# Kernel tuning notes

Hardware: AMD Instinct MI355X
Metric: run time of the kernel (lower is better)

The kernel has to match this reference:

```python
import jax, jax.numpy as jnp
import numpy as np

D = 1024      # input_dim / embed_dim
H = 1024      # hidden_dim
H2 = H // 2
M = 15        # n_masks
NH = 4        # n_heads
B = 8192
LN_EPS = 1e-5


def setup_inputs() -> dict:
    key = jax.random.key(0)
    ks = jax.random.split(key, 16)
    s = 0.02
    return {
        "x": jax.random.normal(ks[0], (B, D), jnp.float32),
        # nn.MultiheadAttention params (torch layout: y = x @ W.T + b)
        "in_proj_w": jax.random.normal(ks[1], (3 * D, D), jnp.float32) * s,
        "in_proj_b": jax.random.normal(ks[2], (3 * D,), jnp.float32) * s,
        "out_proj_w": jax.random.normal(ks[3], (D, D), jnp.float32) * s,
        "out_proj_b": jax.random.normal(ks[4], (D,), jnp.float32) * s,
        # 15 mask MLPs stacked along leading axis (grouped GEMM form)
        "W1": jax.random.normal(ks[5], (M, D, H), jnp.float32) * s,
        "b1": jax.random.normal(ks[6], (M, H), jnp.float32) * s,
        "ln_g": jnp.ones((M, H), jnp.float32),
        "ln_b": jnp.zeros((M, H), jnp.float32),
        "W2": jax.random.normal(ks[7], (M, H, H2), jnp.float32) * s,
        "b2": jax.random.normal(ks[8], (M, H2), jnp.float32) * s,
        "W3": jax.random.normal(ks[9], (M, H2, D), jnp.float32) * s,
        "b3": jax.random.normal(ks[10], (M, D), jnp.float32) * s,
    }


def reference(x, in_proj_w, in_proj_b, out_proj_w, out_proj_b,
              W1, b1, ln_g, ln_b, W2, b2, W3, b3):
    Bn = x.shape[0]
    hd = D // NH
    # --- seq_len=1 self-attention ---
    qkv = x @ in_proj_w.T + in_proj_b                      # [B, 3D]
    q, k, v = jnp.split(qkv, 3, axis=-1)                   # each [B, D]
    qh = q.reshape(Bn, NH, hd)
    kh = k.reshape(Bn, NH, hd)
    vh = v.reshape(Bn, NH, hd)
    scores = jnp.sum(qh * kh, axis=-1) / jnp.sqrt(jnp.float32(hd))  # [B, NH]
    # softmax over kv length = 1 -> all ones (kept for faithfulness)
    w = jax.nn.softmax(scores[..., None], axis=-1)         # [B, NH, 1]
    attn = (w * vh).reshape(Bn, D)                         # [B, D]
    a = attn @ out_proj_w.T + out_proj_b                   # [B, D]
    # --- 15 mask MLPs as one grouped GEMM stack (Dropout is eval->identity) ---
    h1 = jnp.einsum('bd,mdh->mbh', a, W1) + b1[:, None, :]  # [M, B, H]
    mu = jnp.mean(h1, axis=-1, keepdims=True)
    var = jnp.mean(jnp.square(h1 - mu), axis=-1, keepdims=True)
    h1 = (h1 - mu) * jax.lax.rsqrt(var + LN_EPS) * ln_g[:, None, :] + ln_b[:, None, :]
    h1 = jax.nn.gelu(h1, approximate=False)
    h2 = jnp.einsum('mbh,mhk->mbk', h1, W2) + b2[:, None, :]  # [M, B, H2]
    h2 = jax.nn.gelu(h2, approximate=False)
    h3 = jnp.einsum('mbk,mkd->mbd', h2, W3) + b3[:, None, :]  # [M, B, D]
    return jax.nn.sigmoid(h3)                               # [M, B, D]
```

## Files before the change

### kernel.cpp

```cpp
#include <hip/hip_runtime.h>

#define D_  1024
#define H_  1024
#define H2_ 512
#define M_  15
#define B_  8192

typedef __attribute__((ext_vector_type(4))) float f32x4;
typedef __attribute__((ext_vector_type(8))) short short8;

__device__ __forceinline__ unsigned short f2bf(float f) {
  unsigned int u = __float_as_uint(f);
  u += 0x7fffu + ((u >> 16) & 1u);
  return (unsigned short)(u >> 16);
}
__device__ __forceinline__ float bf2f(unsigned int h) {
  return __uint_as_float(h << 16);
}
__device__ __forceinline__ float gelu_exact(float x) {
  return 0.5f * x * (1.0f + erff(x * 0.70710678118654752440f));
}

__global__ void cast_f32_bf16(const float* __restrict__ in, unsigned short* __restrict__ out, int n4) {
  int i = blockIdx.x * blockDim.x + threadIdx.x;
  if (i >= n4) return;
  float4 v = ((const float4*)in)[i];
  ushort4 o;
  o.x = f2bf(v.x); o.y = f2bf(v.y); o.z = f2bf(v.z); o.w = f2bf(v.w);
  ((ushort4*)out)[i] = o;
}

__global__ void transpose_cast(const float* __restrict__ in, unsigned short* __restrict__ out,
                               int K, int N) {
  __shared__ float t[32][33];
  const size_t mo = (size_t)blockIdx.z * K * N;
  in  += mo;
  out += mo;
  const int k0 = blockIdx.x * 32, n0 = blockIdx.y * 32;
  const int tx = threadIdx.x, ty = threadIdx.y;
#pragma unroll
  for (int j = 0; j < 32; j += 8)
    t[ty + j][tx] = in[(size_t)(k0 + ty + j) * N + (n0 + tx)];
  __syncthreads();
#pragma unroll
  for (int j = 0; j < 32; j += 8)
    out[(size_t)(n0 + ty + j) * K + (k0 + tx)] = f2bf(t[tx][ty + j]);
}

template <int EPI>
__launch_bounds__(256, 3)
__global__ void gemm_bt(const unsigned short* __restrict__ A, const unsigned short* __restrict__ Bt,
                        const float* __restrict__ bias, void* __restrict__ Cout,
                        int Mrows, int N, int K,
                        long sA, long sB, long sBias, long sC) {
  __shared__ __align__(16) unsigned short As[128 * 64];
  __shared__ __align__(16) unsigned short Bs[128 * 64];
  const int mz = blockIdx.z;
  A    += (size_t)mz * sA;
  Bt   += (size_t)mz * sB;
  bias += (size_t)mz * sBias;

  const int tid  = threadIdx.x;
  const int w    = tid >> 6;
  const int lane = tid & 63;
  const int row0 = blockIdx.x * 128;
  const int col0 = blockIdx.y * 128;

  f32x4 acc[4][4];
#pragma unroll
  for (int i = 0; i < 4; ++i)
#pragma unroll
    for (int j = 0; j < 4; ++j) acc[i][j] = (f32x4){0.f, 0.f, 0.f, 0.f};

  const int wm = w >> 1, wn = w & 1;
  const int mrow = lane & 15;
  const int kq   = (lane >> 4) << 3;

  for (int k0 = 0; k0 < K; k0 += 64) {
    __syncthreads();
#pragma unroll
    for (int i = 0; i < 4; ++i) {
      const int c  = i * 256 + tid;
      const int m  = c >> 3;
      const int kk = (c & 7) << 3;
      const unsigned short* gA = A  + (size_t)(row0 + m) * K + (k0 + kk);
      const unsigned short* gB = Bt + (size_t)(col0 + m) * K + (k0 + kk);
      const int ldsoff = (i * 256 + w * 64) * 8;
      __builtin_amdgcn_global_load_lds((const __attribute__((address_space(1))) void*)gA,
                                       (__attribute__((address_space(3))) void*)(As + ldsoff),
                                       16, 0, 0);
      __builtin_amdgcn_global_load_lds((const __attribute__((address_space(1))) void*)gB,
                                       (__attribute__((address_space(3))) void*)(Bs + ldsoff),
                                       16, 0, 0);
    }
    __syncthreads();
#pragma unroll
    for (int ki = 0; ki < 64; ki += 32) {
      short8 af[4], bf[4];
#pragma unroll
      for (int f = 0; f < 4; ++f) {
        af[f] = *(const short8*)(As + (wm * 64 + f * 16 + mrow) * 64 + ki + kq);
        bf[f] = *(const short8*)(Bs + (wn * 64 + f * 16 + mrow) * 64 + ki + kq);
      }
#pragma unroll
      for (int fm = 0; fm < 4; ++fm)
#pragma unroll
        for (int fn = 0; fn < 4; ++fn)
          acc[fm][fn] = __builtin_amdgcn_mfma_f32_16x16x32_bf16(af[fm], bf[fn], acc[fm][fn], 0, 0, 0);
    }
  }

  float*          Cf = (float*)Cout          + (size_t)mz * sC;
  unsigned short* Cb = (unsigned short*)Cout + (size_t)mz * sC;
  const int rq = (lane >> 4) << 2;
  const int cl = lane & 15;
#pragma unroll
  for (int fm = 0; fm < 4; ++fm) {
#pragma unroll
    for (int fn = 0; fn < 4; ++fn) {
      const int cc = col0 + wn * 64 + fn * 16 + cl;
      const float bv = bias[cc];
#pragma unroll
      for (int r = 0; r < 4; ++r) {
        const int rr = row0 + wm * 64 + fm * 16 + rq + r;
        float v = acc[fm][fn][r] + bv;
        if (EPI == 2) {
          Cf[(size_t)rr * N + cc] = 1.0f / (1.0f + __expf(-v));
        } else {
          if (EPI == 1) v = gelu_exact(v);
          Cb[(size_t)rr * N + cc] = f2bf(v);
        }
      }
    }
  }
}

#define BAR()   asm volatile("s_barrier" ::: "memory")
#define LGKM0() asm volatile("s_waitcnt lgkmcnt(0)" ::: "memory")
#define VM6()   asm volatile("s_waitcnt vmcnt(6)" ::: "memory")

#define STG_A(bufi, bA, rho0) do {                                                             \
  _Pragma("unroll")                                                                            \
  for (int j_ = 0; j_ < 2; ++j_) {                                                             \
    const int rho_ = (rho0) + j_ * 64 + (tid >> 3);                                            \
    const int gr_  = (((rho_ >> 6) & 1) << 7) | (((rho_ >> 7) & 1) << 6) | (rho_ & 63);        \
    const unsigned short* g_ = (bA) + (size_t)gr_ * K + (((tid & 7) ^ (rho_ & 7)) << 3);       \
    __builtin_amdgcn_global_load_lds((const __attribute__((address_space(1))) void*)g_,        \
        (__attribute__((address_space(3))) void*)(&As[bufi][(rho0) * 64 + (j_ * 512 + w6 * 64) * 8]), \
        16, 0, 0);                                                                             \
  }                                                                                            \
} while (0)

#define STG_B(bufi, bB, rho0) do {                                                             \
  _Pragma("unroll")                                                                            \
  for (int j_ = 0; j_ < 2; ++j_) {                                                             \
    const int rho_ = (rho0) + j_ * 64 + (tid >> 3);                                            \
    const int gc_  = (((rho_ >> 5) & 3) << 6) | (((rho_ >> 7) & 1) << 5) | (rho_ & 31);        \
    const unsigned short* g_ = (bB) + (size_t)gc_ * K + (((tid & 7) ^ (rho_ & 7)) << 3);       \
    __builtin_amdgcn_global_load_lds((const __attribute__((address_space(1))) void*)g_,        \
        (__attribute__((address_space(3))) void*)(&Bs[bufi][(rho0) * 64 + (j_ * 512 + w6 * 64) * 8]), \
        16, 0, 0);                                                                             \
  }                                                                                            \
} while (0)

#define LDA4(bufi, hi) do {                                                                    \
  _Pragma("unroll")                                                                            \
  for (int q_ = 0; q_ < 4; ++q_) {                                                             \
    const int rho_ = ((hi) ? 128 : 0) + wm * 64 + q_ * 16 + lrow;                              \
    a[q_][0] = *(const short8*)&As[bufi][rho_ * 64 + ((lk ^ (rho_ & 7)) << 3)];                \
    a[q_][1] = *(const short8*)&As[bufi][rho_ * 64 + (((4 + lk) ^ (rho_ & 7)) << 3)];          \
  }                                                                                            \
} while (0)

#define LDB2(bufi, hi) do {                                                                    \
  _Pragma("unroll")                                                                            \
  for (int q_ = 0; q_ < 2; ++q_) {                                                             \
    const int rho_ = ((hi) ? 128 : 0) + wn * 32 + q_ * 16 + lrow;                              \
    b[(hi) * 2 + q_][0] = *(const short8*)&Bs[bufi][rho_ * 64 + ((lk ^ (rho_ & 7)) << 3)];     \
    b[(hi) * 2 + q_][1] = *(const short8*)&Bs[bufi][rho_ * 64 + (((4 + lk) ^ (rho_ & 7)) << 3)]; \
  }                                                                                            \
} while (0)

#define MMQ(mh, nh) do {                                                                       \
  __builtin_amdgcn_s_setprio(1);                                                               \
  _Pragma("unroll")                                                                            \
  for (int mq_ = 0; mq_ < 4; ++mq_) {                                                          \
    _Pragma("unroll")                                                                          \
    for (int nq_ = 0; nq_ < 2; ++nq_) {                                                        \
      acc[(mh) * 4 + mq_][(nh) * 2 + nq_] = __builtin_amdgcn_mfma_f32_16x16x32_bf16(           \
          a[mq_][0], b[(nh) * 2 + nq_][0], acc[(mh) * 4 + mq_][(nh) * 2 + nq_], 0, 0, 0);      \
      acc[(mh) * 4 + mq_][(nh) * 2 + nq_] = __builtin_amdgcn_mfma_f32_16x16x32_bf16(           \
          a[mq_][1], b[(nh) * 2 + nq_][1], acc[(mh) * 4 + mq_][(nh) * 2 + nq_], 0, 0, 0);      \
    }                                                                                          \
  }                                                                                            \
  __builtin_amdgcn_s_setprio(0);                                                               \
} while (0)

template <int EPI, int LNT, int LGY>
__launch_bounds__(512, 2)
__global__ void gemm256p(const unsigned short* __restrict__ A, const unsigned short* __restrict__ Bt,
                         const float* __restrict__ bias, void* __restrict__ Cout,
                         int N, int K, long sA, long sB, long sBias, long sC,
                         int ntiles8, int tpb) {
  __shared__ __align__(16) unsigned short As[2][256 * 64];
  __shared__ __align__(16) unsigned short Bs[2][256 * 64];
  const int NT = 1 << LNT, GYm1 = (1 << LGY) - 1;

  const int bid = blockIdx.x;
  const int xcd = bid & 7, lb = bid >> 3;
  const int cb  = xcd * ntiles8;

  const int tid  = threadIdx.x;
  const int w6   = tid >> 6;
  const int lane = tid & 63;
  const int wm   = w6 >> 2;
  const int wn   = w6 & 3;
  const int lrow = lane & 15;
  const int lk   = lane >> 4;

  int t_cur = 0;
  int tix  = cb + lb;
  int row0 = ((tix >> LGY) & 31) << 8;
  int col0 = (tix & GYm1) << 8;
  int mz   = tix >> (LGY + 5);
  const unsigned short* bAc = A  + (size_t)mz * sA + (size_t)row0 * K;
  const unsigned short* bBc = Bt + (size_t)mz * sB + (size_t)col0 * K;

  f32x4 acc[8][4];
#pragma unroll
  for (int i = 0; i < 8; ++i)
#pragma unroll
    for (int j = 0; j < 4; ++j) acc[i][j] = (f32x4){0.f, 0.f, 0.f, 0.f};
  short8 a[4][2], b[4][2];

  STG_A(0, bAc, 0); STG_B(0, bBc, 0); STG_B(0, bBc, 128); STG_A(0, bAc, 128);
  STG_A(1, bAc + 64, 0); STG_B(1, bBc + 64, 0); STG_B(1, bBc + 64, 128);
  VM6(); BAR();

  const int totK = tpb << LNT;
#pragma unroll 1
  for (int T = 0; T < totK; T += 2) {
    const int g2 = (T + 2 < totK) ? T + 2 : totK - 1;
    const int g3 = (T + 3 < totK) ? T + 3 : totK - 1;
    const int t2 = g2 >> LNT, t3 = g3 >> LNT;
    const int tix2 = cb + lb + t2 * 30;
    const int tix3 = cb + lb + t3 * 30;
    const unsigned short* bA2 = A  + (size_t)(tix2 >> (LGY + 5)) * sA
                                   + (size_t)((((tix2 >> LGY) & 31) << 8)) * K + ((g2 & (NT - 1)) << 6);
    const unsigned short* bB2 = Bt + (size_t)(tix2 >> (LGY + 5)) * sB
                                   + (size_t)(((tix2 & GYm1) << 8)) * K + ((g2 & (NT - 1)) << 6);
    const unsigned short* bA3 = A  + (size_t)(tix3 >> (LGY + 5)) * sA
                                   + (size_t)((((tix3 >> LGY) & 31) << 8)) * K + ((g3 & (NT - 1)) << 6);
    const unsigned short* bB3 = Bt + (size_t)(tix3 >> (LGY + 5)) * sB
                                   + (size_t)(((tix3 & GYm1) << 8)) * K + ((g3 & (NT - 1)) << 6);
    const unsigned short* bA1 = bAc + (((T + 1) & (NT - 1)) << 6);

    LDA4(0, 0); LDB2(0, 0);
    STG_A(1, bA1, 128);
    BAR(); LGKM0(); MMQ(0, 0); BAR();
    LDB2(0, 1);
    STG_A(0, bA2, 0);
    BAR(); LGKM0(); MMQ(0, 1); BAR();
    LDA4(0, 1);
    STG_B(0, bB2, 0);
    BAR(); LGKM0(); MMQ(1, 0); BAR();
    STG_B(0, bB2, 128);
    VM6(); BAR(); MMQ(1, 1); BAR();
    LDA4(1, 0); LDB2(1, 0);
    STG_A(0, bA2, 128);
    BAR(); LGKM0(); MMQ(0, 0); BAR();
    LDB2(1, 1);
    STG_A(1, bA3, 0);
    BAR(); LGKM0(); MMQ(0, 1); BAR();
    LDA4(1, 1);
    STG_B(1, bB3, 0);
    BAR(); LGKM0(); MMQ(1, 0); BAR();
    STG_B(1, bB3, 128);
    VM6(); BAR(); MMQ(1, 1); BAR();

    if (((T + 2) & (NT - 1)) == 0) {
      const float* bp = bias + (size_t)mz * sBias;
      float*          Cf = (float*)Cout          + (size_t)mz * sC;
      unsigned short* Cb = (unsigned short*)Cout + (size_t)mz * sC;
      const int rq = (lane >> 4) << 2;
      const int cl = lane & 15;
#pragma unroll
      for (int nf = 0; nf < 4; ++nf) {
        const int cc = col0 + wn * 64 + nf * 16 + cl;
        const float bv = bp[cc];
#pragma unroll
        for (int mf = 0; mf < 8; ++mf) {
#pragma unroll
          for (int r = 0; r < 4; ++r) {
            const int rr = row0 + wm * 128 + mf * 16 + rq + r;
            float v = acc[mf][nf][r] + bv;
            if (EPI == 2) {
              Cf[(size_t)rr * N + cc] = 1.0f / (1.0f + __expf(-v));
            } else {
              if (EPI == 1) v = gelu_exact(v);
              Cb[(size_t)rr * N + cc] = f2bf(v);
            }
          }
        }
      }
#pragma unroll
      for (int i = 0; i < 8; ++i)
#pragma unroll
        for (int j = 0; j < 4; ++j) acc[i][j] = (f32x4){0.f, 0.f, 0.f, 0.f};
      ++t_cur;
      if (t_cur < tpb) {
        tix  = cb + lb + t_cur * 30;
        row0 = ((tix >> LGY) & 31) << 8;
        col0 = (tix & GYm1) << 8;
        mz   = tix >> (LGY + 5);
        bAc  = A  + (size_t)mz * sA + (size_t)row0 * K;
        bBc  = Bt + (size_t)mz * sB + (size_t)col0 * K;
      }
    }
  }
  asm volatile("s_waitcnt vmcnt(0)" ::: "memory");
}

__global__ void ln_gelu(const unsigned short* __restrict__ in, const float* __restrict__ g,
                        const float* __restrict__ bb, unsigned short* __restrict__ out) {
  const int m = blockIdx.y;
  in  += (size_t)m * B_ * H_;
  out += (size_t)m * B_ * H_;
  g   += (size_t)m * H_;
  bb  += (size_t)m * H_;
  const int row = blockIdx.x;
  const int tid = threadIdx.x;
  const unsigned short* rp = in + (size_t)row * H_;
  uint2 u = ((const uint2*)rp)[tid];
  float x0 = bf2f(u.x & 0xffffu);
  float x1 = bf2f(u.x >> 16);
  float x2 = bf2f(u.y & 0xffffu);
  float x3 = bf2f(u.y >> 16);

  float s  = x0 + x1 + x2 + x3;
  float s2 = x0 * x0 + x1 * x1 + x2 * x2 + x3 * x3;
#pragma unroll
  for (int o = 32; o > 0; o >>= 1) {
    s  += __shfl_down(s, o);
    s2 += __shfl_down(s2, o);
  }
  __shared__ float red[10];
  const int w = tid >> 6;
  if ((tid & 63) == 0) { red[w] = s; red[4 + w] = s2; }
  __syncthreads();
  if (tid == 0) {
    float ts = red[0] + red[1] + red[2] + red[3];
    float t2 = red[4] + red[5] + red[6] + red[7];
    float mean = ts * (1.0f / H_);
    float var  = t2 * (1.0f / H_) - mean * mean;
    red[8] = mean;
    red[9] = rsqrtf(var + 1e-5f);
  }
  __syncthreads();
  const float mean = red[8], rstd = red[9];
  const int col = tid * 4;
  float y0 = gelu_exact((x0 - mean) * rstd * g[col + 0] + bb[col + 0]);
  float y1 = gelu_exact((x1 - mean) * rstd * g[col + 1] + bb[col + 1]);
  float y2 = gelu_exact((x2 - mean) * rstd * g[col + 2] + bb[col + 2]);
  float y3 = gelu_exact((x3 - mean) * rstd * g[col + 3] + bb[col + 3]);
  ushort4 o;
  o.x = f2bf(y0); o.y = f2bf(y1); o.z = f2bf(y2); o.w = f2bf(y3);
  ((ushort4*)(out + (size_t)row * H_))[tid] = o;
}

extern "C" void kernel_launch(void* const* d_in, const int* in_sizes, int n_in,
                              void* d_out, int out_size, void* d_ws, size_t ws_size,
                              hipStream_t stream) {
  const float* x   = (const float*)d_in[0];
  const float* ipw = (const float*)d_in[1];
  const float* ipb = (const float*)d_in[2];
  const float* opw = (const float*)d_in[3];
  const float* opb = (const float*)d_in[4];
  const float* W1  = (const float*)d_in[5];
  const float* b1  = (const float*)d_in[6];
  const float* lng = (const float*)d_in[7];
  const float* lnb = (const float*)d_in[8];
  const float* W2  = (const float*)d_in[9];
  const float* b2  = (const float*)d_in[10];
  const float* W3  = (const float*)d_in[11];
  const float* b3  = (const float*)d_in[12];
  float* out = (float*)d_out;

  char* p = (char*)d_ws;
  auto take = [&](size_t bytes) { void* q = (void*)p; p += (bytes + 255) & ~(size_t)255; return q; };
  unsigned short* xb  = (unsigned short*)take((size_t)B_ * D_ * 2);
  unsigned short* wvb = (unsigned short*)take((size_t)D_ * D_ * 2);
  unsigned short* wob = (unsigned short*)take((size_t)D_ * D_ * 2);
  unsigned short* w1t = (unsigned short*)take((size_t)M_ * H_ * D_ * 2);
  unsigned short* w2t = (unsigned short*)take((size_t)M_ * H2_ * H_ * 2);
  unsigned short* w3t = (unsigned short*)take((size_t)M_ * D_ * H2_ * 2);
  unsigned short* vb  = (unsigned short*)take((size_t)B_ * D_ * 2);
  unsigned short* ab  = (unsigned short*)take((size_t)B_ * D_ * 2);
  unsigned short* h1p = (unsigned short*)take((size_t)M_ * B_ * H_ * 2);
  unsigned short* h1a = (unsigned short*)take((size_t)M_ * B_ * H_ * 2);
  unsigned short* h2b = (unsigned short*)take((size_t)M_ * B_ * H2_ * 2);

  cast_f32_bf16<<<dim3((B_ * D_ / 4 + 255) / 256), 256, 0, stream>>>(x, xb, B_ * D_ / 4);
  cast_f32_bf16<<<dim3((D_ * D_ / 4 + 255) / 256), 256, 0, stream>>>(ipw + 2 * D_ * D_, wvb, D_ * D_ / 4);
  cast_f32_bf16<<<dim3((D_ * D_ / 4 + 255) / 256), 256, 0, stream>>>(opw, wob, D_ * D_ / 4);
  transpose_cast<<<dim3(D_ / 32, H_ / 32, M_), dim3(32, 8), 0, stream>>>(W1, w1t, D_, H_);
  transpose_cast<<<dim3(H_ / 32, H2_ / 32, M_), dim3(32, 8), 0, stream>>>(W2, w2t, H_, H2_);
  transpose_cast<<<dim3(H2_ / 32, D_ / 32, M_), dim3(32, 8), 0, stream>>>(W3, w3t, H2_, D_);

  gemm_bt<0><<<dim3(B_ / 128, D_ / 128, 1), 256, 0, stream>>>(
      xb, wvb, ipb + 2 * D_, vb, B_, D_, D_, 0, 0, 0, 0);
  gemm_bt<0><<<dim3(B_ / 128, D_ / 128, 1), 256, 0, stream>>>(
      vb, wob, opb, ab, B_, D_, D_, 0, 0, 0, 0);

  gemm256p<0, 4, 2><<<dim3(240), 512, 0, stream>>>(
      ab, w1t, b1, h1p, H_, D_,
      0, (long)H_ * D_, (long)H_, (long)B_ * H_, 1920 / 8, 8);
  ln_gelu<<<dim3(B_, M_), 256, 0, stream>>>(h1p, lng, lnb, h1a);
  gemm256p<1, 4, 1><<<dim3(240), 512, 0, stream>>>(
      h1a, w2t, b2, h2b, H2_, H_,
      (long)B_ * H_, (long)H2_ * H_, (long)H2_, (long)B_ * H2_, 960 / 8, 4);
  gemm256p<2, 3, 2><<<dim3(240), 512, 0, stream>>>(
      h2b, w3t, b3, out, D_, H2_,
      (long)B_ * H2_, (long)D_ * H2_, (long)D_, (long)B_ * D_, 1920 / 8, 8);
}
```

Before: 1.623 ms.

## Fold V and out projections into one weight; switch grouped GEMM to 32x32 MFMA

```diff
diff --git a/kernel.cpp b/kernel.cpp
--- a/kernel.cpp
+++ b/kernel.cpp
@@ -7,6 +7,7 @@
 #define B_  8192
 
 typedef __attribute__((ext_vector_type(4))) float f32x4;
+typedef __attribute__((ext_vector_type(16))) float f32x16;
 typedef __attribute__((ext_vector_type(8))) short short8;
 
 __device__ __forceinline__ unsigned short f2bf(float f) {
@@ -28,6 +29,22 @@
   ushort4 o;
   o.x = f2bf(v.x); o.y = f2bf(v.y); o.z = f2bf(v.z); o.w = f2bf(v.w);
   ((ushort4*)out)[i] = o;
+}
+
+__global__ void zero_f32(float* __restrict__ p, int n) {
+  int i = blockIdx.x * blockDim.x + threadIdx.x;
+  if (i < n) p[i] = 0.f;
+}
+
+__global__ void bias_fold(const float* __restrict__ opw, const float* __restrict__ bv,
+                          const float* __restrict__ opb, float* __restrict__ bc) {
+  const int o = blockIdx.x;
+  const int l = threadIdx.x;
+  float s = 0.f;
+  for (int d = l; d < D_; d += 64) s += opw[(size_t)o * D_ + d] * bv[d];
+#pragma unroll
+  for (int off = 32; off > 0; off >>= 1) s += __shfl_down(s, off);
+  if (l == 0) bc[o] = s + opb[o];
 }
 
 __global__ void transpose_cast(const float* __restrict__ in, unsigned short* __restrict__ out,
@@ -163,34 +180,33 @@
   }                                                                                            \
 } while (0)
 
-#define LDA4(bufi, hi) do {                                                                    \
+#define LDA32(bufi, mh) do {                                                                   \
   _Pragma("unroll")                                                                            \
-  for (int q_ = 0; q_ < 4; ++q_) {                                                             \
-    const int rho_ = ((hi) ? 128 : 0) + wm * 64 + q_ * 16 + lrow;                              \
-    a[q_][0] = *(const short8*)&As[bufi][rho_ * 64 + ((lk ^ (rho_ & 7)) << 3)];                \
-    a[q_][1] = *(const short8*)&As[bufi][rho_ * 64 + (((4 + lk) ^ (rho_ & 7)) << 3)];          \
+  for (int f2_ = 0; f2_ < 2; ++f2_) {                                                          \
+    const int rho_ = (mh) * 128 + wm * 64 + f2_ * 32 + l31;                                    \
+    _Pragma("unroll")                                                                          \
+    for (int c_ = 0; c_ < 4; ++c_)                                                             \
+      a[f2_][c_] = *(const short8*)&As[bufi][rho_ * 64 + ((((c_ << 1) | lhi) ^ (rho_ & 7)) << 3)]; \
   }                                                                                            \
 } while (0)
 
-#define LDB2(bufi, hi) do {                                                                    \
-  _Pragma("unroll")                                                                            \
-  for (int q_ = 0; q_ < 2; ++q_) {                                                             \
-    const int rho_ = ((hi) ? 128 : 0) + wn * 32 + q_ * 16 + lrow;                              \
-    b[(hi) * 2 + q_][0] = *(const short8*)&Bs[bufi][rho_ * 64 + ((lk ^ (rho_ & 7)) << 3)];     \
-    b[(hi) * 2 + q_][1] = *(const short8*)&Bs[bufi][rho_ * 64 + (((4 + lk) ^ (rho_ & 7)) << 3)]; \
+#define LDB32(bufi, nh) do {                                                                   \
+  {                                                                                            \
+    const int rho_ = (nh) * 128 + wn * 32 + l31;                                               \
+    _Pragma("unroll")                                                                          \
+    for (int c_ = 0; c_ < 4; ++c_)                                                             \
+      b[nh][c_] = *(const short8*)&Bs[bufi][rho_ * 64 + ((((c_ << 1) | lhi) ^ (rho_ & 7)) << 3)]; \
   }                                                                                            \
 } while (0)
 
-#define MMQ(mh, nh) do {                                                                       \
+#define MMQ32(mh, nh) do {                                                                     \
   __builtin_amdgcn_s_setprio(1);                                                               \
   _Pragma("unroll")                                                                            \
-  for (int mq_ = 0; mq_ < 4; ++mq_) {                                                          \
+  for (int c_ = 0; c_ < 4; ++c_) {                                                             \
     _Pragma("unroll")                                                                          \
-    for (int nq_ = 0; nq_ < 2; ++nq_) {                                                        \
-      acc[(mh) * 4 + mq_][(nh) * 2 + nq_] = __builtin_amdgcn_mfma_f32_16x16x32_bf16(           \
-          a[mq_][0], b[(nh) * 2 + nq_][0], acc[(mh) * 4 + mq_][(nh) * 2 + nq_], 0, 0, 0);      \
-      acc[(mh) * 4 + mq_][(nh) * 2 + nq_] = __builtin_amdgcn_mfma_f32_16x16x32_bf16(           \
-          a[mq_][1], b[(nh) * 2 + nq_][1], acc[(mh) * 4 + mq_][(nh) * 2 + nq_], 0, 0, 0);      \
+    for (int f2_ = 0; f2_ < 2; ++f2_) {                                                        \
+      acc[(mh) * 2 + f2_][nh] = __builtin_amdgcn_mfma_f32_32x32x16_bf16(                       \
+          a[f2_][c_], b[nh][c_], acc[(mh) * 2 + f2_][nh], 0, 0, 0);                            \
     }                                                                                          \
   }                                                                                            \
   __builtin_amdgcn_s_setprio(0);                                                               \
@@ -215,8 +231,8 @@
   const int lane = tid & 63;
   const int wm   = w6 >> 2;
   const int wn   = w6 & 3;
-  const int lrow = lane & 15;
-  const int lk   = lane >> 4;
+  const int l31  = lane & 31;
+  const int lhi  = lane >> 5;
 
   int t_cur = 0;
   int tix  = cb + lb;
@@ -226,12 +242,14 @@
   const unsigned short* bAc = A  + (size_t)mz * sA + (size_t)row0 * K;
   const unsigned short* bBc = Bt + (size_t)mz * sB + (size_t)col0 * K;
 
-  f32x4 acc[8][4];
-#pragma unroll
-  for (int i = 0; i < 8; ++i)
-#pragma unroll
-    for (int j = 0; j < 4; ++j) acc[i][j] = (f32x4){0.f, 0.f, 0.f, 0.f};
-  short8 a[4][2], b[4][2];
+  f32x16 acc[4][2];
+#pragma unroll
+  for (int i = 0; i < 4; ++i)
+#pragma unroll
+    for (int j = 0; j < 2; ++j)
+#pragma unroll
+      for (int e = 0; e < 16; ++e) acc[i][j][e] = 0.f;
+  short8 a[2][4], b[2][4];
 
   STG_A(0, bAc, 0); STG_B(0, bBc, 0); STG_B(0, bBc, 128); STG_A(0, bAc, 128);
   STG_A(1, bAc + 64, 0); STG_B(1, bBc + 64, 0); STG_B(1, bBc + 64, 128);
@@ -255,45 +273,43 @@
                                    + (size_t)(((tix3 & GYm1) << 8)) * K + ((g3 & (NT - 1)) << 6);
     const unsigned short* bA1 = bAc + (((T + 1) & (NT - 1)) << 6);
 
-    LDA4(0, 0); LDB2(0, 0);
+    LDA32(0, 0); LDB32(0, 0);
     STG_A(1, bA1, 128);
-    BAR(); LGKM0(); MMQ(0, 0); BAR();
-    LDB2(0, 1);
+    BAR(); LGKM0(); MMQ32(0, 0); BAR();
+    LDB32(0, 1);
     STG_A(0, bA2, 0);
-    BAR(); LGKM0(); MMQ(0, 1); BAR();
-    LDA4(0, 1);
+    BAR(); LGKM0(); MMQ32(0, 1); BAR();
+    LDA32(0, 1);
     STG_B(0, bB2, 0);
-    BAR(); LGKM0(); MMQ(1, 0); BAR();
+    BAR(); LGKM0(); MMQ32(1, 0); BAR();
     STG_B(0, bB2, 128);
-    VM6(); BAR(); MMQ(1, 1); BAR();
-    LDA4(1, 0); LDB2(1, 0);
+    VM6(); BAR(); MMQ32(1, 1); BAR();
+    LDA32(1, 0); LDB32(1, 0);
     STG_A(0, bA2, 128);
-    BAR(); LGKM0(); MMQ(0, 0); BAR();
-    LDB2(1, 1);
+    BAR(); LGKM0(); MMQ32(0, 0); BAR();
+    LDB32(1, 1);
     STG_A(1, bA3, 0);
-    BAR(); LGKM0(); MMQ(0, 1); BAR();
-    LDA4(1, 1);
+    BAR(); LGKM0(); MMQ32(0, 1); BAR();
+    LDA32(1, 1);
     STG_B(1, bB3, 0);
-    BAR(); LGKM0(); MMQ(1, 0); BAR();
+    BAR(); LGKM0(); MMQ32(1, 0); BAR();
     STG_B(1, bB3, 128);
-    VM6(); BAR(); MMQ(1, 1); BAR();
+    VM6(); BAR(); MMQ32(1, 1); BAR();
 
     if (((T + 2) & (NT - 1)) == 0) {
       const float* bp = bias + (size_t)mz * sBias;
       float*          Cf = (float*)Cout          + (size_t)mz * sC;
       unsigned short* Cb = (unsigned short*)Cout + (size_t)mz * sC;
-      const int rq = (lane >> 4) << 2;
-      const int cl = lane & 15;
-#pragma unroll
-      for (int nf = 0; nf < 4; ++nf) {
-        const int cc = col0 + wn * 64 + nf * 16 + cl;
+#pragma unroll
+      for (int nf = 0; nf < 2; ++nf) {
+        const int cc = col0 + wn * 64 + nf * 32 + l31;
         const float bv = bp[cc];
 #pragma unroll
-        for (int mf = 0; mf < 8; ++mf) {
-#pragma unroll
-          for (int r = 0; r < 4; ++r) {
-            const int rr = row0 + wm * 128 + mf * 16 + rq + r;
-            float v = acc[mf][nf][r] + bv;
+        for (int mf = 0; mf < 4; ++mf) {
+#pragma unroll
+          for (int reg = 0; reg < 16; ++reg) {
+            const int rr = row0 + wm * 128 + mf * 32 + (reg & 3) + ((reg >> 2) << 3) + (lhi << 2);
+            float v = acc[mf][nf][reg] + bv;
             if (EPI == 2) {
               Cf[(size_t)rr * N + cc] = 1.0f / (1.0f + __expf(-v));
             } else {
@@ -304,9 +320,11 @@
         }
       }
 #pragma unroll
-      for (int i = 0; i < 8; ++i)
-#pragma unroll
-        for (int j = 0; j < 4; ++j) acc[i][j] = (f32x4){0.f, 0.f, 0.f, 0.f};
+      for (int i = 0; i < 4; ++i)
+#pragma unroll
+        for (int j = 0; j < 2; ++j)
+#pragma unroll
+          for (int e = 0; e < 16; ++e) acc[i][j][e] = 0.f;
       ++t_cur;
       if (t_cur < tpb) {
         tix  = cb + lb + t_cur * 30;
@@ -389,28 +407,32 @@
   char* p = (char*)d_ws;
   auto take = [&](size_t bytes) { void* q = (void*)p; p += (bytes + 255) & ~(size_t)255; return q; };
   unsigned short* xb  = (unsigned short*)take((size_t)B_ * D_ * 2);
-  unsigned short* wvb = (unsigned short*)take((size_t)D_ * D_ * 2);
   unsigned short* wob = (unsigned short*)take((size_t)D_ * D_ * 2);
+  unsigned short* wvt = (unsigned short*)take((size_t)D_ * D_ * 2);
+  unsigned short* wcb = (unsigned short*)take((size_t)D_ * D_ * 2);
+  float*          zb  = (float*)take((size_t)D_ * 4);
+  float*          bc  = (float*)take((size_t)D_ * 4);
   unsigned short* w1t = (unsigned short*)take((size_t)M_ * H_ * D_ * 2);
   unsigned short* w2t = (unsigned short*)take((size_t)M_ * H2_ * H_ * 2);
   unsigned short* w3t = (unsigned short*)take((size_t)M_ * D_ * H2_ * 2);
-  unsigned short* vb  = (unsigned short*)take((size_t)B_ * D_ * 2);
   unsigned short* ab  = (unsigned short*)take((size_t)B_ * D_ * 2);
   unsigned short* h1p = (unsigned short*)take((size_t)M_ * B_ * H_ * 2);
   unsigned short* h1a = (unsigned short*)take((size_t)M_ * B_ * H_ * 2);
   unsigned short* h2b = (unsigned short*)take((size_t)M_ * B_ * H2_ * 2);
 
   cast_f32_bf16<<<dim3((B_ * D_ / 4 + 255) / 256), 256, 0, stream>>>(x, xb, B_ * D_ / 4);
-  cast_f32_bf16<<<dim3((D_ * D_ / 4 + 255) / 256), 256, 0, stream>>>(ipw + 2 * D_ * D_, wvb, D_ * D_ / 4);
   cast_f32_bf16<<<dim3((D_ * D_ / 4 + 255) / 256), 256, 0, stream>>>(opw, wob, D_ * D_ / 4);
+  transpose_cast<<<dim3(D_ / 32, D_ / 32, 1), dim3(32, 8), 0, stream>>>(ipw + 2 * D_ * D_, wvt, D_, D_);
   transpose_cast<<<dim3(D_ / 32, H_ / 32, M_), dim3(32, 8), 0, stream>>>(W1, w1t, D_, H_);
   transpose_cast<<<dim3(H_ / 32, H2_ / 32, M_), dim3(32, 8), 0, stream>>>(W2, w2t, H_, H2_);
   transpose_cast<<<dim3(H2_ / 32, D_ / 32, M_), dim3(32, 8), 0, stream>>>(W3, w3t, H2_, D_);
-
+  zero_f32<<<dim3(4), 256, 0, stream>>>(zb, D_);
+
+  gemm_bt<0><<<dim3(D_ / 128, D_ / 128, 1), 256, 0, stream>>>(
+      wob, wvt, zb, wcb, D_, D_, D_, 0, 0, 0, 0);
+  bias_fold<<<dim3(D_), 64, 0, stream>>>(opw, ipb + 2 * D_, opb, bc);
   gemm_bt<0><<<dim3(B_ / 128, D_ / 128, 1), 256, 0, stream>>>(
-      xb, wvb, ipb + 2 * D_, vb, B_, D_, D_, 0, 0, 0, 0);
-  gemm_bt<0><<<dim3(B_ / 128, D_ / 128, 1), 256, 0, stream>>>(
-      vb, wob, opb, ab, B_, D_, D_, 0, 0, 0, 0);
+      xb, wcb, bc, ab, B_, D_, D_, 0, 0, 0, 0);
 
   gemm256p<0, 4, 2><<<dim3(240), 512, 0, stream>>>(
       ab, w1t, b1, h1p, H_, D_,
```

Result: no change. 1.655 ms (+2.0%).
